# Performance work log

Measured on AMD Instinct MI355X. Metric: run time of the kernel, lower is better.

## Reference

```python
import jax, jax.numpy as jnp
import numpy as np

B, Q, HID = 16, 1, 1024
LH, LD = 32, 128            # large num heads / large head dim
BLOCK, NBPS = 16, 64        # cache block size, blocks per sequence
NBLK, MAXLEN = B * NBPS, NBPS * BLOCK
ROPE_BASE = 10000.0


def setup_inputs() -> dict:
    key = jax.random.key(0)
    ks = jax.random.split(key, 6)
    hidden_states = jax.random.normal(ks[0], (B, Q, HID), jnp.float32)
    q_proj_w = jax.random.normal(ks[1], (LH * LD, HID), jnp.float32) * 0.02
    o_proj_w = jax.random.normal(ks[2], (HID, LH * LD), jnp.float32) * 0.02
    k_cache = jax.random.normal(ks[3], (NBLK, LH, BLOCK, LD), jnp.float32)
    v_cache = jax.random.normal(ks[4], (NBLK, LH, BLOCK, LD), jnp.float32)
    # each sequence owns NBPS distinct cache blocks
    block_tables = jnp.arange(NBLK, dtype=jnp.int32).reshape(B, NBPS)
    sequence_lengths = jax.random.randint(ks[5], (B,), 1, MAXLEN + 1).astype(jnp.int32)
    position_ids = (sequence_lengths - 1).astype(jnp.int32).reshape(B, Q)
    return dict(hidden_states=hidden_states, q_proj_w=q_proj_w, o_proj_w=o_proj_w,
                k_cache=k_cache, v_cache=v_cache, block_tables=block_tables,
                sequence_lengths=sequence_lengths, position_ids=position_ids,
                n_spec_tokens=5)


def _rotate_half(x):
    h = x.shape[-1] // 2
    return jnp.concatenate([-x[..., h:], x[..., :h]], axis=-1)


def reference(hidden_states, q_proj_w, o_proj_w, k_cache, v_cache,
              block_tables, sequence_lengths, position_ids, n_spec_tokens):
    # q projection -> [B, Q, LH, LD]
    q = (hidden_states @ q_proj_w.T).reshape(B, Q, LH, LD)
    # RoPE at positions shifted by n_spec_tokens
    pos = (position_ids + n_spec_tokens).astype(jnp.float32)              # [B, Q]
    inv_freq = 1.0 / (ROPE_BASE ** (jnp.arange(0, LD, 2, dtype=jnp.float32) / LD))
    freqs = pos[..., None] * inv_freq                                      # [B, Q, LD/2]
    emb = jnp.concatenate([freqs, freqs], axis=-1)                         # [B, Q, LD]
    cos = jnp.cos(emb)[:, :, None, :]
    sin = jnp.sin(emb)[:, :, None, :]
    q = q * cos + _rotate_half(q) * sin
    q = q.reshape(B * Q, LH, LD)  # q_len == 1 -> [B, LH, LD]
    # gather paged KV: [B, NBPS, LH, BLOCK, LD] -> [B, L, LH, LD]
    k = k_cache[block_tables].transpose(0, 1, 3, 2, 4).reshape(B, MAXLEN, LH, LD)
    v = v_cache[block_tables].transpose(0, 1, 3, 2, 4).reshape(B, MAXLEN, LH, LD)
    scale = float(1.0 / np.sqrt(LD))
    scores = jnp.einsum('bhd,blhd->bhl', q, k) * scale                     # [B, LH, L]
    valid = jnp.arange(MAXLEN)[None, :] < sequence_lengths[:, None]        # [B, L]
    scores = jnp.where(valid[:, None, :], scores, -jnp.inf)
    attn = jax.nn.softmax(scores, axis=-1)
    out = jnp.einsum('bhl,blhd->bhd', attn, v).reshape(B, Q, LH * LD)
    return out @ o_proj_w.T                                                # [B, Q, HID]
```

## Files before the change

### kernel.cpp

```cpp
#include <hip/hip_runtime.h>
#include <hip/hip_bf16.h>
#include <math.h>

#define B_   16
#define HID_ 1024
#define LH_  32
#define LD_  128
#define BLOCK_ 16
#define NBPS_  64
#define MAXLEN_ 1024
#define SPLIT_ 4
#define CHUNK_ (MAXLEN_ / SPLIT_)

typedef float vf4 __attribute__((ext_vector_type(4)));

__global__ __launch_bounds__(256) void qproj_rope_kernel(const float* __restrict__ hs,
                                                         const float* __restrict__ w,
                                                         const int* __restrict__ pid,
                                                         const int* __restrict__ nsp,
                                                         float* __restrict__ q) {
    int t = threadIdx.x;
    int h = blockIdx.x >> 3;
    int g = blockIdx.x & 7;
    __shared__ float shs[16 * 1024];
    __shared__ float ssum[16][16];
    {
        const vf4* src = (const vf4*)hs;
        vf4* dst = (vf4*)shs;
        for (int i = t; i < 4096; i += 256) dst[i] = src[i];
    }
    int j  = t >> 5;
    int sl = t & 31;
    int r0 = h * 128 + g * 8 + j;
    int r1 = r0 + 64;
    vf4 w0[8], w1[8];
#pragma unroll
    for (int s = 0; s < 8; ++s) {
        w0[s] = *(const vf4*)&w[(size_t)r0 * HID_ + s * 128 + sl * 4];
        w1[s] = *(const vf4*)&w[(size_t)r1 * HID_ + s * 128 + sl * 4];
    }
    __syncthreads();
    for (int b = 0; b < B_; ++b) {
        float p0 = 0.f, p1 = 0.f;
#pragma unroll
        for (int s = 0; s < 8; ++s) {
            vf4 a = *(const vf4*)&shs[b * 1024 + s * 128 + sl * 4];
            p0 += w0[s].x*a.x + w0[s].y*a.y + w0[s].z*a.z + w0[s].w*a.w;
            p1 += w1[s].x*a.x + w1[s].y*a.y + w1[s].z*a.z + w1[s].w*a.w;
        }
#pragma unroll
        for (int o = 1; o < 32; o <<= 1) { p0 += __shfl_xor(p0, o); p1 += __shfl_xor(p1, o); }
        if (sl == 0) { ssum[j][b] = p0; ssum[j + 8][b] = p1; }
    }
    __syncthreads();
    if (t < 128) {
        int jj = t >> 4;
        int b  = t & 15;
        int d  = g * 8 + jj;
        double x0 = (double)ssum[jj][b];
        double x1 = (double)ssum[jj + 8][b];
        double pos = (double)(pid[b] + nsp[0]);
        double inv_freq = 1.0 / pow(10000.0, (double)d * (1.0 / 64.0));
        double f = pos * inv_freq;
        double cs = cos(f), sn = sin(f);
        const double scale = 0.08838834764831845;
        int base = b * 4096 + h * LD_ + d;
        q[base]      = (float)((x0 * cs - x1 * sn) * scale);
        q[base + 64] = (float)((x1 * cs + x0 * sn) * scale);
    }
}

__global__ __launch_bounds__(256) void attn_kernel(const float* __restrict__ q,
                                                   const float* __restrict__ kc,
                                                   const float* __restrict__ vc,
                                                   const int* __restrict__ btab,
                                                   const int* __restrict__ slen,
                                                   float* __restrict__ pml,
                                                   float* __restrict__ pacc) {
    int c = blockIdx.x, h = blockIdx.y, b = blockIdx.z;
    int L = slen[b];
    int start = c * CHUNK_;
    int bh = b * LH_ + h;
    int pbase = bh * SPLIT_ + c;
    int t = threadIdx.x;

    if (start >= L) {
        if (t < 128) pacc[(size_t)pbase * 128 + t] = 0.f;
        if (t == 0) { pml[pbase * 2] = -INFINITY; pml[pbase * 2 + 1] = 0.f; }
        return;
    }

    int lane = t & 63, wv = t >> 6;
    int sg = lane >> 4;
    int lg = lane & 15;
    int d0 = lg * 8;
    const float* qp = q + (size_t)bh * LD_ + d0;
    vf4 qa = *(const vf4*)qp;
    vf4 qb = *(const vf4*)(qp + 4);

    int end = min(start + CHUNK_, L);
    float m = -INFINITY, l = 0.f;
    float acc[8];
#pragma unroll
    for (int k = 0; k < 8; ++k) acc[k] = 0.f;

#pragma unroll 2
    for (int pos = start + wv * 4 + sg; pos < end; pos += 16) {
        int blk = btab[b * NBPS_ + (pos >> 4)];
        size_t off = (((size_t)blk * LH_ + h) * BLOCK_ + (pos & 15)) * LD_ + d0;
        vf4 k0 = *(const vf4*)(kc + off);
        vf4 k1 = *(const vf4*)(kc + off + 4);
        vf4 v0 = *(const vf4*)(vc + off);
        vf4 v1 = *(const vf4*)(vc + off + 4);

        float dot = qa.x*k0.x + qa.y*k0.y + qa.z*k0.z + qa.w*k0.w
                  + qb.x*k1.x + qb.y*k1.y + qb.z*k1.z + qb.w*k1.w;
#pragma unroll
        for (int o = 1; o < 16; o <<= 1) dot += __shfl_xor(dot, o);

        float mn = fmaxf(m, dot);
        float r = (m >= mn) ? 1.f : __expf(m - mn);
        float p = __expf(dot - mn);
        l = l * r + p;
        acc[0] = acc[0]*r + p*v0.x;  acc[1] = acc[1]*r + p*v0.y;
        acc[2] = acc[2]*r + p*v0.z;  acc[3] = acc[3]*r + p*v0.w;
        acc[4] = acc[4]*r + p*v1.x;  acc[5] = acc[5]*r + p*v1.y;
        acc[6] = acc[6]*r + p*v1.z;  acc[7] = acc[7]*r + p*v1.w;
        m = mn;
    }

#pragma unroll
    for (int o = 16; o < 64; o <<= 1) {
        float m2 = __shfl_xor(m, o), l2 = __shfl_xor(l, o);
        float a2[8];
#pragma unroll
        for (int k = 0; k < 8; ++k) a2[k] = __shfl_xor(acc[k], o);
        float mn = fmaxf(m, m2);
        float ra = (m  >= mn) ? 1.f : __expf(m  - mn);
        float rb = (m2 >= mn) ? 1.f : __expf(m2 - mn);
        l = l * ra + l2 * rb;
#pragma unroll
        for (int k = 0; k < 8; ++k) acc[k] = acc[k]*ra + a2[k]*rb;
        m = mn;
    }

    __shared__ float sm[4], sl_[4], sacc[4][128];
    if (lane < 16) {
#pragma unroll
        for (int k = 0; k < 8; ++k) sacc[wv][d0 + k] = acc[k];
        if (lane == 0) { sm[wv] = m; sl_[wv] = l; }
    }
    __syncthreads();

    if (t < 64) {
        float M = fmaxf(fmaxf(sm[0], sm[1]), fmaxf(sm[2], sm[3]));
        int d = t * 2;
        float lt = 0.f, o0 = 0.f, o1 = 0.f;
#pragma unroll
        for (int w2 = 0; w2 < 4; ++w2) {
            float mw = sm[w2];
            float e = (mw >= M) ? 1.f : __expf(mw - M);
            lt += e * sl_[w2];
            o0 += e * sacc[w2][d];
            o1 += e * sacc[w2][d + 1];
        }
        pacc[(size_t)pbase * 128 + d]     = o0;
        pacc[(size_t)pbase * 128 + d + 1] = o1;
        if (t == 0) { pml[pbase * 2] = M; pml[pbase * 2 + 1] = lt; }
    }
}

__global__ __launch_bounds__(64) void combine_kernel(const float* __restrict__ pml,
                                                     const float* __restrict__ pacc,
                                                     float* __restrict__ attn) {
    int bh = blockIdx.x;
    int lane = threadIdx.x;
    float M = -INFINITY;
#pragma unroll
    for (int c = 0; c < SPLIT_; ++c) M = fmaxf(M, pml[(bh * SPLIT_ + c) * 2]);
    int d = lane * 2;
    float lt = 0.f, o0 = 0.f, o1 = 0.f;
#pragma unroll
    for (int c = 0; c < SPLIT_; ++c) {
        float mc = pml[(bh * SPLIT_ + c) * 2];
        float e = (mc >= M) ? 1.f : __expf(mc - M);
        lt += e * pml[(bh * SPLIT_ + c) * 2 + 1];
        o0 += e * pacc[((size_t)bh * SPLIT_ + c) * 128 + d];
        o1 += e * pacc[((size_t)bh * SPLIT_ + c) * 128 + d + 1];
    }
    float inv = 1.f / lt;
    attn[(size_t)bh * LD_ + d]     = o0 * inv;
    attn[(size_t)bh * LD_ + d + 1] = o1 * inv;
}

__global__ __launch_bounds__(256) void oproj_kernel(const float* __restrict__ attn,
                                                    const float* __restrict__ w,
                                                    float* __restrict__ out) {
    int t = threadIdx.x;
    int row0 = blockIdx.x * 4;
    float wr[4][16];
#pragma unroll
    for (int r = 0; r < 4; ++r)
#pragma unroll
        for (int s = 0; s < 16; ++s)
            wr[r][s] = w[(size_t)(row0 + r) * 4096 + t + 256 * s];

    int lane = t & 63, wv = t >> 6;
    __shared__ float lds[16][4][4];
    for (int b = 0; b < B_; ++b) {
        float p[4] = {0.f, 0.f, 0.f, 0.f};
#pragma unroll
        for (int s = 0; s < 16; ++s) {
            float a = attn[b * 4096 + t + 256 * s];
#pragma unroll
            for (int r = 0; r < 4; ++r) p[r] += wr[r][s] * a;
        }
#pragma unroll
        for (int off = 32; off; off >>= 1)
#pragma unroll
            for (int r = 0; r < 4; ++r) p[r] += __shfl_xor(p[r], off);
        if (lane == 0)
#pragma unroll
            for (int r = 0; r < 4; ++r) lds[b][wv][r] = p[r];
    }
    __syncthreads();
    if (t < 64) {
        int b = t >> 2, r = t & 3;
        out[b * HID_ + row0 + r] = lds[b][0][r] + lds[b][1][r] + lds[b][2][r] + lds[b][3][r];
    }
}

extern "C" void kernel_launch(void* const* d_in, const int* in_sizes, int n_in,
                              void* d_out, int out_size, void* d_ws, size_t ws_size,
                              hipStream_t stream) {
    const float* hs   = (const float*)d_in[0];
    const float* qw   = (const float*)d_in[1];
    const float* ow   = (const float*)d_in[2];
    const float* kc   = (const float*)d_in[3];
    const float* vc   = (const float*)d_in[4];
    const int*   btab = (const int*)d_in[5];
    const int*   slen = (const int*)d_in[6];
    const int*   pid  = (const int*)d_in[7];
    const int*   nsp  = (const int*)d_in[8];
    float* out = (float*)d_out;
    float* ws  = (float*)d_ws;

    float* q_ws    = ws;
    float* attn_ws = ws + 65536;
    float* pml     = ws + 131072;
    float* pacc    = ws + 139264;

    qproj_rope_kernel<<<256, 256, 0, stream>>>(hs, qw, pid, nsp, q_ws);
    attn_kernel<<<dim3(SPLIT_, LH_, B_), 256, 0, stream>>>(q_ws, kc, vc, btab, slen, pml, pacc);
    combine_kernel<<<B_ * LH_, 64, 0, stream>>>(pml, pacc, attn_ws);
    oproj_kernel<<<256, 256, 0, stream>>>(attn_ws, ow, out);
}
```

Measured before the change: 118.0 us.

## Fully unroll split-K attention into two-pass softmax with batched K/V loads

Replaces the per-position online-softmax loop with a fully unrolled structure. All 16 block-table entries are preloaded into registers, and all 16 K rows are loaded and their dot products computed. A single max and exp pass follows, then the V rows are accumulated without rescaling. This exposes many independent loads for memory-level parallelism and removes per-step rescale exps. Invalid positions are clamped to the last valid row and masked to -inf, with -3e38 guards to avoid NaN. It costs more registers and fetches redundant rows for short chunks.

```diff
diff --git a/kernel.cpp b/kernel.cpp
--- a/kernel.cpp
+++ b/kernel.cpp
@@ -99,67 +99,93 @@
     vf4 qb = *(const vf4*)(qp + 4);
 
     int end = min(start + CHUNK_, L);
-    float m = -INFINITY, l = 0.f;
-    float acc[8];
-#pragma unroll
-    for (int k = 0; k < 8; ++k) acc[k] = 0.f;
-
-#pragma unroll 2
-    for (int pos = start + wv * 4 + sg; pos < end; pos += 16) {
-        int blk = btab[b * NBPS_ + (pos >> 4)];
-        size_t off = (((size_t)blk * LH_ + h) * BLOCK_ + (pos & 15)) * LD_ + d0;
+    int nvalid = end - start;
+    int li = (nvalid - 1) >> 4;
+    int lp = (nvalid - 1) & 15;
+
+    int blkr[16];
+#pragma unroll
+    for (int i = 0; i < 16; ++i) blkr[i] = btab[b * NBPS_ + c * 16 + i];
+
+    int po = wv * 4 + sg;
+
+    float dots[16];
+#pragma unroll
+    for (int i = 0; i < 16; ++i) {
+        bool valid = (po + 16 * i) < nvalid;
+        int ii = valid ? i : li;
+        int pc = valid ? po : lp;
+        size_t off = (((size_t)blkr[ii] * LH_ + h) * BLOCK_ + pc) * LD_ + d0;
         vf4 k0 = *(const vf4*)(kc + off);
         vf4 k1 = *(const vf4*)(kc + off + 4);
+        float dot = qa.x*k0.x + qa.y*k0.y + qa.z*k0.z + qa.w*k0.w
+                  + qb.x*k1.x + qb.y*k1.y + qb.z*k1.z + qb.w*k1.w;
+#pragma unroll
+        for (int o = 1; o < 16; o <<= 1) dot += __shfl_xor(dot, o);
+        dots[i] = valid ? dot : -INFINITY;
+    }
+
+    float m = dots[0];
+#pragma unroll
+    for (int i = 1; i < 16; ++i) m = fmaxf(m, dots[i]);
+    float mm = fmaxf(m, -3.0e38f);
+    float l = 0.f;
+#pragma unroll
+    for (int i = 0; i < 16; ++i) {
+        dots[i] = __expf(dots[i] - mm);
+        l += dots[i];
+    }
+
+    float acc[8];
+#pragma unroll
+    for (int k = 0; k < 8; ++k) acc[k] = 0.f;
+#pragma unroll
+    for (int i = 0; i < 16; ++i) {
+        bool valid = (po + 16 * i) < nvalid;
+        int ii = valid ? i : li;
+        int pc = valid ? po : lp;
+        size_t off = (((size_t)blkr[ii] * LH_ + h) * BLOCK_ + pc) * LD_ + d0;
         vf4 v0 = *(const vf4*)(vc + off);
         vf4 v1 = *(const vf4*)(vc + off + 4);
-
-        float dot = qa.x*k0.x + qa.y*k0.y + qa.z*k0.z + qa.w*k0.w
-                  + qb.x*k1.x + qb.y*k1.y + qb.z*k1.z + qb.w*k1.w;
-#pragma unroll
-        for (int o = 1; o < 16; o <<= 1) dot += __shfl_xor(dot, o);
-
-        float mn = fmaxf(m, dot);
-        float r = (m >= mn) ? 1.f : __expf(m - mn);
-        float p = __expf(dot - mn);
-        l = l * r + p;
-        acc[0] = acc[0]*r + p*v0.x;  acc[1] = acc[1]*r + p*v0.y;
-        acc[2] = acc[2]*r + p*v0.z;  acc[3] = acc[3]*r + p*v0.w;
-        acc[4] = acc[4]*r + p*v1.x;  acc[5] = acc[5]*r + p*v1.y;
-        acc[6] = acc[6]*r + p*v1.z;  acc[7] = acc[7]*r + p*v1.w;
-        m = mn;
-    }
-
+        float p = dots[i];
+        acc[0] += p*v0.x;  acc[1] += p*v0.y;  acc[2] += p*v0.z;  acc[3] += p*v0.w;
+        acc[4] += p*v1.x;  acc[5] += p*v1.y;  acc[6] += p*v1.z;  acc[7] += p*v1.w;
+    }
+
+    float mg = m;
 #pragma unroll
     for (int o = 16; o < 64; o <<= 1) {
-        float m2 = __shfl_xor(m, o), l2 = __shfl_xor(l, o);
+        float m2 = __shfl_xor(mg, o), l2 = __shfl_xor(l, o);
         float a2[8];
 #pragma unroll
         for (int k = 0; k < 8; ++k) a2[k] = __shfl_xor(acc[k], o);
-        float mn = fmaxf(m, m2);
-        float ra = (m  >= mn) ? 1.f : __expf(m  - mn);
-        float rb = (m2 >= mn) ? 1.f : __expf(m2 - mn);
+        float mn = fmaxf(mg, m2);
+        float mnG = fmaxf(mn, -3.0e38f);
+        float ra = (mg >= mn) ? 1.f : __expf(fmaxf(mg, -3.0e38f) - mnG);
+        float rb = (m2 >= mn) ? 1.f : __expf(fmaxf(m2, -3.0e38f) - mnG);
         l = l * ra + l2 * rb;
 #pragma unroll
         for (int k = 0; k < 8; ++k) acc[k] = acc[k]*ra + a2[k]*rb;
-        m = mn;
+        mg = mn;
     }
 
     __shared__ float sm[4], sl_[4], sacc[4][128];
     if (lane < 16) {
 #pragma unroll
         for (int k = 0; k < 8; ++k) sacc[wv][d0 + k] = acc[k];
-        if (lane == 0) { sm[wv] = m; sl_[wv] = l; }
+        if (lane == 0) { sm[wv] = mg; sl_[wv] = l; }
     }
     __syncthreads();
 
     if (t < 64) {
         float M = fmaxf(fmaxf(sm[0], sm[1]), fmaxf(sm[2], sm[3]));
+        float MG = fmaxf(M, -3.0e38f);
         int d = t * 2;
         float lt = 0.f, o0 = 0.f, o1 = 0.f;
 #pragma unroll
         for (int w2 = 0; w2 < 4; ++w2) {
             float mw = sm[w2];
-            float e = (mw >= M) ? 1.f : __expf(mw - M);
+            float e = (mw >= M) ? 1.f : __expf(fmaxf(mw, -3.0e38f) - MG);
             lt += e * sl_[w2];
             o0 += e * sacc[w2][d];
             o1 += e * sacc[w2][d + 1];
```

Result: slower. 129.7 us (+10.0%).

## Use persistent attention blocks with atomic work queue and finer KV split

Applied to the files above, without the earlier changes.

Raises the sequence split from 4 to 16 chunks and replaces the fixed grid with 2048 persistent blocks that pull (batch, head, chunk) work items from a global atomic counter, reset by the q-projection kernel. The aim is to balance load across CUs when sequence lengths vary widely, and to expose more parallelism for short sequences. In exchange it adds an atomic and extra barriers per item, and gives the combine kernel four times as many partials to merge.

```diff
diff --git a/kernel.cpp b/kernel.cpp
--- a/kernel.cpp
+++ b/kernel.cpp
@@ -9,8 +9,10 @@
 #define BLOCK_ 16
 #define NBPS_  64
 #define MAXLEN_ 1024
-#define SPLIT_ 4
+#define SPLIT_ 16
 #define CHUNK_ (MAXLEN_ / SPLIT_)
+#define NITEMS_ (SPLIT_ * LH_ * B_)
+#define NBLOCKS_ 2048
 
 typedef float vf4 __attribute__((ext_vector_type(4)));
 
@@ -18,8 +20,10 @@
                                                          const float* __restrict__ w,
                                                          const int* __restrict__ pid,
                                                          const int* __restrict__ nsp,
-                                                         float* __restrict__ q) {
+                                                         float* __restrict__ q,
+                                                         int* __restrict__ cnt) {
     int t = threadIdx.x;
+    if (blockIdx.x == 0 && t == 0) *cnt = 0;
     int h = blockIdx.x >> 3;
     int g = blockIdx.x & 7;
     __shared__ float shs[16 * 1024];
@@ -76,97 +80,113 @@
                                                    const int* __restrict__ btab,
                                                    const int* __restrict__ slen,
                                                    float* __restrict__ pml,
-                                                   float* __restrict__ pacc) {
-    int c = blockIdx.x, h = blockIdx.y, b = blockIdx.z;
-    int L = slen[b];
-    int start = c * CHUNK_;
-    int bh = b * LH_ + h;
-    int pbase = bh * SPLIT_ + c;
+                                                   float* __restrict__ pacc,
+                                                   int* __restrict__ cnt) {
     int t = threadIdx.x;
-
-    if (start >= L) {
-        if (t < 128) pacc[(size_t)pbase * 128 + t] = 0.f;
-        if (t == 0) { pml[pbase * 2] = -INFINITY; pml[pbase * 2 + 1] = 0.f; }
-        return;
-    }
-
     int lane = t & 63, wv = t >> 6;
     int sg = lane >> 4;
     int lg = lane & 15;
     int d0 = lg * 8;
-    const float* qp = q + (size_t)bh * LD_ + d0;
-    vf4 qa = *(const vf4*)qp;
-    vf4 qb = *(const vf4*)(qp + 4);
-
-    int end = min(start + CHUNK_, L);
-    float m = -INFINITY, l = 0.f;
-    float acc[8];
-#pragma unroll
-    for (int k = 0; k < 8; ++k) acc[k] = 0.f;
+    int po = wv * 4 + sg;
+
+    __shared__ int sitem;
+    __shared__ float sm[4], sl_[4], sacc[4][128];
+
+    while (true) {
+        if (t == 0) sitem = atomicAdd(cnt, 1);
+        __syncthreads();
+        int item = sitem;
+        if (item >= NITEMS_) break;
+
+        int c = item & (SPLIT_ - 1);
+        int h = (item >> 4) & (LH_ - 1);
+        int b = item >> 9;
+        int L = slen[b];
+        int start = c * CHUNK_;
+        int bh = b * LH_ + h;
+        int pbase = bh * SPLIT_ + c;
+
+        if (start >= L) {
+            if (t < 128) pacc[(size_t)pbase * 128 + t] = 0.f;
+            if (t == 0) { pml[pbase * 2] = -INFINITY; pml[pbase * 2 + 1] = 0.f; }
+            __syncthreads();
+            continue;
+        }
+
+        const float* qp = q + (size_t)bh * LD_ + d0;
+        vf4 qa = *(const vf4*)qp;
+        vf4 qb = *(const vf4*)(qp + 4);
+
+        int end = min(start + CHUNK_, L);
+        float m = -INFINITY, l = 0.f;
+        float acc[8];
+#pragma unroll
+        for (int k = 0; k < 8; ++k) acc[k] = 0.f;
 
 #pragma unroll 2
-    for (int pos = start + wv * 4 + sg; pos < end; pos += 16) {
-        int blk = btab[b * NBPS_ + (pos >> 4)];
-        size_t off = (((size_t)blk * LH_ + h) * BLOCK_ + (pos & 15)) * LD_ + d0;
-        vf4 k0 = *(const vf4*)(kc + off);
-        vf4 k1 = *(const vf4*)(kc + off + 4);
-        vf4 v0 = *(const vf4*)(vc + off);
-        vf4 v1 = *(const vf4*)(vc + off + 4);
-
-        float dot = qa.x*k0.x + qa.y*k0.y + qa.z*k0.z + qa.w*k0.w
-                  + qb.x*k1.x + qb.y*k1.y + qb.z*k1.z + qb.w*k1.w;
-#pragma unroll
-        for (int o = 1; o < 16; o <<= 1) dot += __shfl_xor(dot, o);
-
-        float mn = fmaxf(m, dot);
-        float r = (m >= mn) ? 1.f : __expf(m - mn);
-        float p = __expf(dot - mn);
-        l = l * r + p;
-        acc[0] = acc[0]*r + p*v0.x;  acc[1] = acc[1]*r + p*v0.y;
-        acc[2] = acc[2]*r + p*v0.z;  acc[3] = acc[3]*r + p*v0.w;
-        acc[4] = acc[4]*r + p*v1.x;  acc[5] = acc[5]*r + p*v1.y;
-        acc[6] = acc[6]*r + p*v1.z;  acc[7] = acc[7]*r + p*v1.w;
-        m = mn;
-    }
-
-#pragma unroll
-    for (int o = 16; o < 64; o <<= 1) {
-        float m2 = __shfl_xor(m, o), l2 = __shfl_xor(l, o);
-        float a2[8];
-#pragma unroll
-        for (int k = 0; k < 8; ++k) a2[k] = __shfl_xor(acc[k], o);
-        float mn = fmaxf(m, m2);
-        float ra = (m  >= mn) ? 1.f : __expf(m  - mn);
-        float rb = (m2 >= mn) ? 1.f : __expf(m2 - mn);
-        l = l * ra + l2 * rb;
-#pragma unroll
-        for (int k = 0; k < 8; ++k) acc[k] = acc[k]*ra + a2[k]*rb;
-        m = mn;
-    }
-
-    __shared__ float sm[4], sl_[4], sacc[4][128];
-    if (lane < 16) {
-#pragma unroll
-        for (int k = 0; k < 8; ++k) sacc[wv][d0 + k] = acc[k];
-        if (lane == 0) { sm[wv] = m; sl_[wv] = l; }
-    }
-    __syncthreads();
-
-    if (t < 64) {
-        float M = fmaxf(fmaxf(sm[0], sm[1]), fmaxf(sm[2], sm[3]));
-        int d = t * 2;
-        float lt = 0.f, o0 = 0.f, o1 = 0.f;
-#pragma unroll
-        for (int w2 = 0; w2 < 4; ++w2) {
-            float mw = sm[w2];
-            float e = (mw >= M) ? 1.f : __expf(mw - M);
-            lt += e * sl_[w2];
-            o0 += e * sacc[w2][d];
-            o1 += e * sacc[w2][d + 1];
-        }
-        pacc[(size_t)pbase * 128 + d]     = o0;
-        pacc[(size_t)pbase * 128 + d + 1] = o1;
-        if (t == 0) { pml[pbase * 2] = M; pml[pbase * 2 + 1] = lt; }
+        for (int pos = start + po; pos < end; pos += 16) {
+            int blk = btab[b * NBPS_ + (pos >> 4)];
+            size_t off = (((size_t)blk * LH_ + h) * BLOCK_ + (pos & 15)) * LD_ + d0;
+            vf4 k0 = *(const vf4*)(kc + off);
+            vf4 k1 = *(const vf4*)(kc + off + 4);
+            vf4 v0 = *(const vf4*)(vc + off);
+            vf4 v1 = *(const vf4*)(vc + off + 4);
+
+            float dot = qa.x*k0.x + qa.y*k0.y + qa.z*k0.z + qa.w*k0.w
+                      + qb.x*k1.x + qb.y*k1.y + qb.z*k1.z + qb.w*k1.w;
+#pragma unroll
+            for (int o = 1; o < 16; o <<= 1) dot += __shfl_xor(dot, o);
+
+            float mn = fmaxf(m, dot);
+            float r = (m >= mn) ? 1.f : __expf(m - mn);
+            float p = __expf(dot - mn);
+            l = l * r + p;
+            acc[0] = acc[0]*r + p*v0.x;  acc[1] = acc[1]*r + p*v0.y;
+            acc[2] = acc[2]*r + p*v0.z;  acc[3] = acc[3]*r + p*v0.w;
+            acc[4] = acc[4]*r + p*v1.x;  acc[5] = acc[5]*r + p*v1.y;
+            acc[6] = acc[6]*r + p*v1.z;  acc[7] = acc[7]*r + p*v1.w;
+            m = mn;
+        }
+
+#pragma unroll
+        for (int o = 16; o < 64; o <<= 1) {
+            float m2 = __shfl_xor(m, o), l2 = __shfl_xor(l, o);
+            float a2[8];
+#pragma unroll
+            for (int k = 0; k < 8; ++k) a2[k] = __shfl_xor(acc[k], o);
+            float mn = fmaxf(m, m2);
+            float ra = (m  >= mn) ? 1.f : __expf(m  - mn);
+            float rb = (m2 >= mn) ? 1.f : __expf(m2 - mn);
+            l = l * ra + l2 * rb;
+#pragma unroll
+            for (int k = 0; k < 8; ++k) acc[k] = acc[k]*ra + a2[k]*rb;
+            m = mn;
+        }
+
+        if (lane < 16) {
+#pragma unroll
+            for (int k = 0; k < 8; ++k) sacc[wv][d0 + k] = acc[k];
+            if (lane == 0) { sm[wv] = m; sl_[wv] = l; }
+        }
+        __syncthreads();
+
+        if (t < 64) {
+            float M = fmaxf(fmaxf(sm[0], sm[1]), fmaxf(sm[2], sm[3]));
+            int d = t * 2;
+            float lt = 0.f, o0 = 0.f, o1 = 0.f;
+#pragma unroll
+            for (int w2 = 0; w2 < 4; ++w2) {
+                float mw = sm[w2];
+                float e = (mw >= M) ? 1.f : __expf(mw - M);
+                lt += e * sl_[w2];
+                o0 += e * sacc[w2][d];
+                o1 += e * sacc[w2][d + 1];
+            }
+            pacc[(size_t)pbase * 128 + d]     = o0;
+            pacc[(size_t)pbase * 128 + d + 1] = o1;
+            if (t == 0) { pml[pbase * 2] = M; pml[pbase * 2 + 1] = lt; }
+        }
+        __syncthreads();
     }
 }
 
@@ -247,11 +267,12 @@
 
     float* q_ws    = ws;
     float* attn_ws = ws + 65536;
-    float* pml     = ws + 131072;
-    float* pacc    = ws + 139264;
-
-    qproj_rope_kernel<<<256, 256, 0, stream>>>(hs, qw, pid, nsp, q_ws);
-    attn_kernel<<<dim3(SPLIT_, LH_, B_), 256, 0, stream>>>(q_ws, kc, vc, btab, slen, pml, pacc);
+    int*   cnt     = (int*)(ws + 131072);
+    float* pml     = ws + 131328;
+    float* pacc    = ws + 147712;
+
+    qproj_rope_kernel<<<256, 256, 0, stream>>>(hs, qw, pid, nsp, q_ws, cnt);
+    attn_kernel<<<NBLOCKS_, 256, 0, stream>>>(q_ws, kc, vc, btab, slen, pml, pacc, cnt);
     combine_kernel<<<B_ * LH_, 64, 0, stream>>>(pml, pacc, attn_ws);
     oproj_kernel<<<256, 256, 0, stream>>>(attn_ws, ow, out);
 }
```

Result: slower. 174.5 us (+48.0%).
